# Kernel tuning notes

Hardware: AMD Instinct MI355X
Metric: run time of the kernel (lower is better)

## Reference

```python
import jax, jax.numpy as jnp
import numpy as np

NUM_LEVELS = 16
LEVEL_DIM = 2
BASE_RES = 16
END_RES = 2048
TABLE = 1 << 19  # log2_hashmap_size = 19
DIVIDE = 1.5
FV = 256  # feature_vector_size
H = 256   # hidden width
N = 262144
_scale = np.exp((np.log(END_RES) - np.log(BASE_RES)) / (NUM_LEVELS - 1))
RES = [int(np.ceil(BASE_RES * _scale ** l)) for l in range(NUM_LEVELS)]


def hash_encode(x, tables):
    # x: [N,3], assumed in [-1,1]; map to [0,1] as instant-ngp does
    x01 = jnp.clip((x + 1.0) * 0.5, 0.0, 1.0)
    feats = []
    for l in range(NUM_LEVELS):
        res = RES[l]
        pos = x01 * (res - 1)                      # [N,3]
        p0 = jnp.floor(pos).astype(jnp.int32)
        w = pos - p0                               # trilinear weights
        dense = (res + 1) ** 3 <= TABLE            # static per level
        acc = jnp.zeros((x.shape[0], LEVEL_DIM), x.dtype)
        for c in range(8):                         # 8 cube corners
            off = np.array([(c >> d) & 1 for d in range(3)], dtype=np.int32)
            p = jnp.minimum(p0 + off, res)
            if dense:
                idx = p[:, 0] + (res + 1) * (p[:, 1] + (res + 1) * p[:, 2])
            else:
                pu = p.astype(jnp.uint32)
                idx = (pu[:, 0] ^ (pu[:, 1] * np.uint32(2654435761)) ^ (pu[:, 2] * np.uint32(805459861))) & np.uint32(TABLE - 1)
                idx = idx.astype(jnp.int32)
            wc = jnp.prod(jnp.where(off == 1, w, 1.0 - w), axis=-1, keepdims=True)
            acc = acc + wc * tables[l][idx]
        feats.append(acc)
    return jnp.concatenate(feats, -1)              # [N, 32]


def softplus100(x):
    # torch.nn.Softplus(beta=100)
    return jnp.logaddexp(0.0, 100.0 * x) / 100.0


def mlp(h, W0, b0, W1, b1, W2, b2):
    h = softplus100(h @ W0.T + b0)
    h = softplus100(h @ W1.T + b1)
    return h @ W2.T + b2


def setup_inputs() -> dict:
    key = jax.random.key(0)
    ks = jax.random.split(key, 12)
    GF = NUM_LEVELS * LEVEL_DIM
    d_c = 3 + GF           # coarse MLP input dim (35)
    d_f = 3 + GF + FV      # fine MLP input dim (291)

    def w(k, o, i):
        return jax.random.normal(k, (o, i), jnp.float32) * np.float32(1.0 / np.sqrt(i))

    return {
        'x': jax.random.uniform(ks[0], (N, 3), jnp.float32, -1.0, 1.0),
        'c_tables': jax.random.normal(ks[1], (NUM_LEVELS, TABLE, LEVEL_DIM), jnp.float32) * 1e-2,
        'c_W0': w(ks[2], H, d_c), 'c_b0': jnp.zeros((H,), jnp.float32),
        'c_W1': w(ks[3], H, H),   'c_b1': jnp.zeros((H,), jnp.float32),
        'c_W2': w(ks[4], 1 + FV, H), 'c_b2': jnp.zeros((1 + FV,), jnp.float32),
        'f_tables': jax.random.normal(ks[5], (NUM_LEVELS, TABLE, LEVEL_DIM), jnp.float32) * 1e-2,
        'f_W0': w(ks[6], H, d_f), 'f_b0': jnp.zeros((H,), jnp.float32),
        'f_W1': w(ks[7], H, H),   'f_b1': jnp.zeros((H,), jnp.float32),
        'f_W2': w(ks[8], 1 + FV, H), 'f_b2': jnp.zeros((1 + FV,), jnp.float32),
    }


def reference(x, c_tables, c_W0, c_b0, c_W1, c_b1, c_W2, c_b2,
              f_tables, f_W0, f_b0, f_W1, f_b1, f_W2, f_b2):
    # coarse network: input = [x, hash_feat]
    c_feat = hash_encode(x / DIVIDE, c_tables)
    c_in = jnp.concatenate([x, c_feat], -1)
    c_out = mlp(c_in, c_W0, c_b0, c_W1, c_b1, c_W2, c_b2)  # [N, 1+FV]
    c_fv = c_out[:, 1:]
    # fine network with concat_coarse_feature: input = [x, hash_feat, c_fv]
    f_feat = hash_encode(x / DIVIDE, f_tables)
    f_in = jnp.concatenate([x, f_feat, c_fv], -1)
    f_out = mlp(f_in, f_W0, f_b0, f_W1, f_b1, f_W2, f_b2)  # [N, 1+FV]
    # COMBINE: (c_sdf + f_sdf, c_feature + f_feature) == c_out + f_out
    return c_out + f_out
```

## Files before the change

### kernel.cpp

```cpp
#include <hip/hip_runtime.h>
#include <cmath>

#define NLEV 16
#define TBLSZ 524288
#define TMASK 524287u
#define STR 66
#define ROWS 291
#define NPB 64

typedef short short8 __attribute__((ext_vector_type(8)));
typedef float f32x4 __attribute__((ext_vector_type(4)));
typedef unsigned int u32;
typedef unsigned short u16;

struct EncParams { int res[NLEV]; unsigned dense_mask; };

__device__ __host__ __forceinline__ u32 bf16_rtne_bits(float x) {
  union { float f; u32 u; } c; c.f = x;
  return (c.u + 0x7fffu + ((c.u >> 16) & 1u)) >> 16;
}

__device__ __forceinline__ float softplus100(float x) {
  float t = 100.0f * x;
  return (fmaxf(t, 0.0f) + log1pf(expf(-fabsf(t)))) * 0.01f;
}

__device__ __forceinline__ u32 pack_hl(float x) {
  u32 hi = bf16_rtne_bits(x);
  float r = x - __uint_as_float(hi << 16);
  u32 lo = bf16_rtne_bits(r);
  return hi | (lo << 16);
}

struct AF { short8 h, l; };

template<int KT, int IN>
__device__ __forceinline__ void load_a(const u32* hb, int p, int kq, AF* af) {
  #pragma unroll
  for (int t = 0; t < KT; ++t) {
    u32 pk[8];
    const bool tail = ((t + 1) * 32 > IN);
    #pragma unroll
    for (int e = 0; e < 8; ++e) {
      const int k = t * 32 + kq + e;
      if (tail) {
        const int row = (k < IN) ? k : (IN - 1);
        const u32 v = hb[row * STR + p];
        pk[e] = (k < IN) ? v : 0u;
      } else {
        pk[e] = hb[k * STR + p];
      }
    }
    union { u32 u[4]; short8 v; } ch, cl;
    #pragma unroll
    for (int q = 0; q < 4; ++q) {
      ch.u[q] = __builtin_amdgcn_perm(pk[2 * q + 1], pk[2 * q], 0x05040100u);
      cl.u[q] = __builtin_amdgcn_perm(pk[2 * q + 1], pk[2 * q], 0x07060302u);
    }
    af[t].h = ch.v;
    af[t].l = cl.v;
  }
}

template<int KT, int NT, int IN, class Post>
__device__ __forceinline__ void layer(const u32* __restrict__ hb,
                                      const u16* __restrict__ wf,
                                      const float* __restrict__ bias,
                                      int p, int kq, int l, Post&& post) {
  AF af[KT];
  load_a<KT, IN>(hb, p, kq, af);
  __syncthreads();
  const short8* __restrict__ wp0 = ((const short8*)wf) + (l << 1);
  #pragma unroll 2
  for (int n = 0; n < NT; ++n) {
    const int j = n * 16 + (l & 15);
    const float bv = bias[j];
    f32x4 acc = {bv, bv, bv, bv};
    const short8* wp = wp0 + (size_t)(n * KT) * 128;
    #pragma unroll
    for (int t = 0; t < KT; ++t) {
      const short8 bh = wp[t * 128];
      const short8 bl = wp[t * 128 + 1];
      acc = __builtin_amdgcn_mfma_f32_16x16x32_bf16(af[t].h, bh, acc, 0, 0, 0);
      acc = __builtin_amdgcn_mfma_f32_16x16x32_bf16(af[t].h, bl, acc, 0, 0, 0);
      acc = __builtin_amdgcn_mfma_f32_16x16x32_bf16(af[t].l, bh, acc, 0, 0, 0);
    }
    post(n, j, acc);
  }
}

__global__ __launch_bounds__(256)
void prep_weights(const float* __restrict__ s0, const float* __restrict__ s1,
                  const float* __restrict__ s2, const float* __restrict__ s3,
                  const float* __restrict__ s4, const float* __restrict__ s5,
                  u16* __restrict__ ws) {
  const int O[6]   = {256, 256, 257, 256, 256, 257};
  const int K[6]   = {35, 256, 256, 291, 256, 256};
  const int KT[6]  = {2, 8, 8, 10, 8, 8};
  const int NE[6]  = {16384, 65536, 69632, 81920, 65536, 69632};
  const int OFF[6] = {0, 32768, 163840, 303104, 466944, 598016};
  const float* S[6] = {s0, s1, s2, s3, s4, s5};
  int t = blockIdx.x * 256 + threadIdx.x;
  #pragma unroll
  for (int L = 0; L < 6; ++L) {
    if (t < NE[L]) {
      const int e = t & 7, lane = (t >> 3) & 63, f = t >> 9;
      const int kt = f % KT[L], nt = f / KT[L];
      const int j = nt * 16 + (lane & 15);
      const int k = kt * 32 + ((lane >> 4) << 3) + e;
      const float v = (j < O[L] && k < K[L]) ? S[L][(size_t)j * K[L] + k] : 0.0f;
      const u32 hi = bf16_rtne_bits(v);
      const float r = v - __uint_as_float(hi << 16);
      const u32 lo = bf16_rtne_bits(r);
      u16* d = ws + OFF[L] + (size_t)f * 1024 + (size_t)lane * 16;
      d[e] = (u16)hi;
      d[8 + e] = (u16)lo;
      return;
    }
    t -= NE[L];
  }
}

__global__ __launch_bounds__(256, 2)
void fused_ingp(const float* __restrict__ x,
                const float* __restrict__ ctab, const float* __restrict__ cb0,
                const float* __restrict__ cb1, const float* __restrict__ cb2,
                const float* __restrict__ ftab, const float* __restrict__ fb0,
                const float* __restrict__ fb1, const float* __restrict__ fb2,
                const u16* __restrict__ cW0p, const u16* __restrict__ cW1p,
                const u16* __restrict__ cW2p, const u16* __restrict__ fW0p,
                const u16* __restrict__ fW1p, const u16* __restrict__ fW2p,
                float* __restrict__ out, EncParams ep) {
  __shared__ u32 hb[ROWS * STR];
  const int tid = threadIdx.x;
  const int l = tid & 63;
  const int g = __builtin_amdgcn_readfirstlane(tid >> 6);
  const int pbase = blockIdx.x * NPB;
  const int pt = pbase + l;
  const int p = g * 16 + (l & 15);
  const int kq = (l >> 4) << 3;
  const int colb = g * 16 + ((l >> 4) << 2);

  const float* xp = x + (size_t)3 * pt;
  const float x0 = xp[0], x1 = xp[1], x2 = xp[2];
  const float q0 = fminf(fmaxf((x0 / 1.5f + 1.0f) * 0.5f, 0.0f), 1.0f);
  const float q1 = fminf(fmaxf((x1 / 1.5f + 1.0f) * 0.5f, 0.0f), 1.0f);
  const float q2 = fminf(fmaxf((x2 / 1.5f + 1.0f) * 0.5f, 0.0f), 1.0f);

  if (g == 0) {
    const u32 px0 = pack_hl(x0), px1 = pack_hl(x1), px2 = pack_hl(x2);
    hb[0 * STR + l] = px0; hb[1 * STR + l] = px1; hb[2 * STR + l] = px2;
    hb[288 * STR + l] = px0; hb[289 * STR + l] = px1; hb[290 * STR + l] = px2;
  }

  #pragma unroll
  for (int il = 0; il < 4; ++il) {
    const int lv = g * 4 + il;
    const int res = ep.res[lv];
    const bool dense = (ep.dense_mask >> lv) & 1;
    const float rf = (float)(res - 1);
    const float px = q0 * rf, py = q1 * rf, pz = q2 * rf;
    const int ix = (int)floorf(px), iy = (int)floorf(py), iz = (int)floorf(pz);
    const float wx = px - (float)ix, wy = py - (float)iy, wz = pz - (float)iz;
    float ca0 = 0.f, ca1 = 0.f, fa0 = 0.f, fa1 = 0.f;
    const float* ct = ctab + (size_t)lv * TBLSZ * 2;
    const float* ft = ftab + (size_t)lv * TBLSZ * 2;
    #pragma unroll
    for (int c = 0; c < 8; ++c) {
      const int ox = c & 1, oy = (c >> 1) & 1, oz = (c >> 2) & 1;
      const int cx = min(ix + ox, res), cy = min(iy + oy, res), cz = min(iz + oz, res);
      unsigned idx;
      if (dense) idx = (unsigned)(cx + (res + 1) * (cy + (res + 1) * cz));
      else idx = (((unsigned)cx) ^ ((unsigned)cy * 2654435761u) ^ ((unsigned)cz * 805459861u)) & TMASK;
      const float wc = (ox ? wx : 1.0f - wx) * (oy ? wy : 1.0f - wy) * (oz ? wz : 1.0f - wz);
      const float2 cv = *(const float2*)(ct + (size_t)idx * 2);
      const float2 fv = *(const float2*)(ft + (size_t)idx * 2);
      ca0 = fmaf(wc, cv.x, ca0); ca1 = fmaf(wc, cv.y, ca1);
      fa0 = fmaf(wc, fv.x, fa0); fa1 = fmaf(wc, fv.y, fa1);
    }
    hb[(3 + 2 * lv) * STR + l] = pack_hl(ca0);
    hb[(4 + 2 * lv) * STR + l] = pack_hl(ca1);
    hb[(256 + 2 * lv) * STR + l] = pack_hl(fa0);
    hb[(257 + 2 * lv) * STR + l] = pack_hl(fa1);
  }
  __syncthreads();

  auto post_act = [&](int n, int j, f32x4 a) {
    (void)n;
    #pragma unroll
    for (int r = 0; r < 4; ++r)
      hb[j * STR + colb + r] = pack_hl(softplus100(a[r]));
  };

  layer<2, 16, 35>(hb, cW0p, cb0, p, kq, l, post_act);
  __syncthreads();
  layer<8, 16, 256>(hb, cW1p, cb1, p, kq, l, post_act);
  __syncthreads();

  f32x4 ck[17];
  {
    AF af[8];
    load_a<8, 256>(hb, p, kq, af);
    __syncthreads();
    for (int r = g; r < 35; r += 4) {
      const int src = (r < 3) ? (288 + r) : (253 + r);
      hb[r * STR + l] = hb[src * STR + l];
    }
    __syncthreads();
    const short8* __restrict__ wp0 = ((const short8*)cW2p) + (l << 1);
    #pragma unroll
    for (int n = 0; n < 17; ++n) {
      const int j = n * 16 + (l & 15);
      const float bv = (j < 257) ? cb2[j] : 0.0f;
      f32x4 a = {bv, bv, bv, bv};
      const short8* wp = wp0 + (size_t)(n * 8) * 128;
      #pragma unroll
      for (int t = 0; t < 8; ++t) {
        const short8 bh = wp[t * 128];
        const short8 bl = wp[t * 128 + 1];
        a = __builtin_amdgcn_mfma_f32_16x16x32_bf16(af[t].h, bh, a, 0, 0, 0);
        a = __builtin_amdgcn_mfma_f32_16x16x32_bf16(af[t].h, bl, a, 0, 0, 0);
        a = __builtin_amdgcn_mfma_f32_16x16x32_bf16(af[t].l, bh, a, 0, 0, 0);
      }
      ck[n] = a;
      if (j >= 1 && j <= 256) {
        #pragma unroll
        for (int r = 0; r < 4; ++r)
          hb[(34 + j) * STR + colb + r] = pack_hl(a[r]);
      }
    }
  }
  __syncthreads();

  layer<10, 16, 291>(hb, fW0p, fb0, p, kq, l, post_act);
  __syncthreads();
  layer<8, 16, 256>(hb, fW1p, fb1, p, kq, l, post_act);
  __syncthreads();

  {
    AF af[8];
    load_a<8, 256>(hb, p, kq, af);
    __syncthreads();
    float* hbf = (float*)hb;
    const short8* __restrict__ wp0 = ((const short8*)fW2p) + (l << 1);
    #pragma unroll
    for (int n = 0; n < 17; ++n) {
      const int j = n * 16 + (l & 15);
      const float bv = (j < 257) ? fb2[j] : 0.0f;
      f32x4 a = {bv, bv, bv, bv};
      const short8* wp = wp0 + (size_t)(n * 8) * 128;
      #pragma unroll
      for (int t = 0; t < 8; ++t) {
        const short8 bh = wp[t * 128];
        const short8 bl = wp[t * 128 + 1];
        a = __builtin_amdgcn_mfma_f32_16x16x32_bf16(af[t].h, bh, a, 0, 0, 0);
        a = __builtin_amdgcn_mfma_f32_16x16x32_bf16(af[t].h, bl, a, 0, 0, 0);
        a = __builtin_amdgcn_mfma_f32_16x16x32_bf16(af[t].l, bh, a, 0, 0, 0);
      }
      if (j <= 256) {
        #pragma unroll
        for (int r = 0; r < 4; ++r)
          hbf[j * STR + colb + r] = ck[n][r] + a[r];
      }
    }
  }
  __syncthreads();

  const float* hbf = (const float*)hb;
  const size_t obase = (size_t)pbase * 257;
  for (int idx = tid; idx < NPB * 257; idx += 256) {
    const int pp = idx / 257;
    const int j = idx - pp * 257;
    out[obase + idx] = hbf[j * STR + pp];
  }
}

extern "C" void kernel_launch(void* const* d_in, const int* in_sizes, int n_in,
                              void* d_out, int out_size, void* d_ws, size_t ws_size,
                              hipStream_t stream) {
  (void)n_in; (void)out_size; (void)ws_size;
  EncParams ep;
  const double sc = std::exp((std::log(2048.0) - std::log(16.0)) / 15.0);
  unsigned dm = 0;
  for (int l = 0; l < NLEV; ++l) {
    const int r = (int)std::ceil(16.0 * std::pow(sc, (double)l));
    ep.res[l] = r;
    const long long rp = (long long)r + 1;
    if (rp * rp * rp <= (long long)TBLSZ) dm |= (1u << l);
  }
  ep.dense_mask = dm;

  const float* X    = (const float*)d_in[0];
  const float* ctab = (const float*)d_in[1];
  const float* cW0  = (const float*)d_in[2];
  const float* cb0  = (const float*)d_in[3];
  const float* cW1  = (const float*)d_in[4];
  const float* cb1  = (const float*)d_in[5];
  const float* cW2  = (const float*)d_in[6];
  const float* cb2  = (const float*)d_in[7];
  const float* ftab = (const float*)d_in[8];
  const float* fW0  = (const float*)d_in[9];
  const float* fb0  = (const float*)d_in[10];
  const float* fW1  = (const float*)d_in[11];
  const float* fb1  = (const float*)d_in[12];
  const float* fW2  = (const float*)d_in[13];
  const float* fb2  = (const float*)d_in[14];

  u16* ws = (u16*)d_ws;
  u16* cW0p = ws + 0;
  u16* cW1p = ws + 32768;
  u16* cW2p = ws + 163840;
  u16* fW0p = ws + 303104;
  u16* fW1p = ws + 466944;
  u16* fW2p = ws + 598016;

  prep_weights<<<dim3(1440), dim3(256), 0, stream>>>(cW0, cW1, cW2, fW0, fW1, fW2, ws);

  const int N = in_sizes[0] / 3;
  fused_ingp<<<dim3(N / NPB), dim3(256), 0, stream>>>(
      X, ctab, cb0, cb1, cb2, ftab, fb0, fb1, fb2,
      cW0p, cW1p, cW2p, fW0p, fW1p, fW2p,
      (float*)d_out, ep);
}
```

Baseline: 2.327 ms.

## Split MLP tiles 2x2 across waves and spill coarse outputs to global

Each of the four waves now computes 32 points by half of the output columns, instead of 16 points by all columns. Each B-weight fragment is therefore reused across two A tiles, which halves weight loads per MFMA. The coarse output previously lived in a 17-entry register array (ck). It is now packed as hi/lo bf16 into the output buffer with nontemporal stores and read back at the final combine, which lowers register pressure. The cost is an extra global write and read of the coarse result, and a slightly lossy hi/lo bf16 round trip for the coarse output.

```diff
diff --git a/kernel.cpp b/kernel.cpp
--- a/kernel.cpp
+++ b/kernel.cpp
@@ -30,6 +30,9 @@
   float r = x - __uint_as_float(hi << 16);
   u32 lo = bf16_rtne_bits(r);
   return hi | (lo << 16);
+}
+__device__ __forceinline__ float unpack_hl(u32 v) {
+  return __uint_as_float(v << 16) + __uint_as_float(v & 0xFFFF0000u);
 }
 
 struct AF { short8 h, l; };
@@ -62,30 +65,35 @@
   }
 }
 
-template<int KT, int NT, int IN, class Post>
-__device__ __forceinline__ void layer(const u32* __restrict__ hb,
-                                      const u16* __restrict__ wf,
-                                      const float* __restrict__ bias,
-                                      int p, int kq, int l, Post&& post) {
-  AF af[KT];
-  load_a<KT, IN>(hb, p, kq, af);
+template<int KT, int NTW, int IN, class Post>
+__device__ __forceinline__ void layer2(const u32* __restrict__ hb,
+                                       const u16* __restrict__ wf,
+                                       const float* __restrict__ bias,
+                                       int nbase, int p0, int kq, int l, Post&& post) {
+  AF a0[KT], a1[KT];
+  load_a<KT, IN>(hb, p0, kq, a0);
+  load_a<KT, IN>(hb, p0 + 16, kq, a1);
   __syncthreads();
   const short8* __restrict__ wp0 = ((const short8*)wf) + (l << 1);
   #pragma unroll 2
-  for (int n = 0; n < NT; ++n) {
-    const int j = n * 16 + (l & 15);
+  for (int n = 0; n < NTW; ++n) {
+    const int nn = nbase + n;
+    const int j = nn * 16 + (l & 15);
     const float bv = bias[j];
-    f32x4 acc = {bv, bv, bv, bv};
-    const short8* wp = wp0 + (size_t)(n * KT) * 128;
+    f32x4 acc0 = {bv, bv, bv, bv}, acc1 = acc0;
+    const short8* wp = wp0 + (size_t)(nn * KT) * 128;
     #pragma unroll
     for (int t = 0; t < KT; ++t) {
       const short8 bh = wp[t * 128];
       const short8 bl = wp[t * 128 + 1];
-      acc = __builtin_amdgcn_mfma_f32_16x16x32_bf16(af[t].h, bh, acc, 0, 0, 0);
-      acc = __builtin_amdgcn_mfma_f32_16x16x32_bf16(af[t].h, bl, acc, 0, 0, 0);
-      acc = __builtin_amdgcn_mfma_f32_16x16x32_bf16(af[t].l, bh, acc, 0, 0, 0);
-    }
-    post(n, j, acc);
+      acc0 = __builtin_amdgcn_mfma_f32_16x16x32_bf16(a0[t].h, bh, acc0, 0, 0, 0);
+      acc1 = __builtin_amdgcn_mfma_f32_16x16x32_bf16(a1[t].h, bh, acc1, 0, 0, 0);
+      acc0 = __builtin_amdgcn_mfma_f32_16x16x32_bf16(a0[t].h, bl, acc0, 0, 0, 0);
+      acc1 = __builtin_amdgcn_mfma_f32_16x16x32_bf16(a1[t].h, bl, acc1, 0, 0, 0);
+      acc0 = __builtin_amdgcn_mfma_f32_16x16x32_bf16(a0[t].l, bh, acc0, 0, 0, 0);
+      acc1 = __builtin_amdgcn_mfma_f32_16x16x32_bf16(a1[t].l, bh, acc1, 0, 0, 0);
+    }
+    post(j, acc0, acc1);
   }
 }
 
@@ -135,11 +143,13 @@
   const int tid = threadIdx.x;
   const int l = tid & 63;
   const int g = __builtin_amdgcn_readfirstlane(tid >> 6);
+  const int mg = g & 1;
+  const int ng = g >> 1;
   const int pbase = blockIdx.x * NPB;
   const int pt = pbase + l;
-  const int p = g * 16 + (l & 15);
+  const int p0 = mg * 32 + (l & 15);
   const int kq = (l >> 4) << 3;
-  const int colb = g * 16 + ((l >> 4) << 2);
+  const int cb = mg * 32 + ((l >> 4) << 2);
 
   const float* xp = x + (size_t)3 * pt;
   const float x0 = xp[0], x1 = xp[1], x2 = xp[2];
@@ -185,22 +195,24 @@
   }
   __syncthreads();
 
-  auto post_act = [&](int n, int j, f32x4 a) {
-    (void)n;
-    #pragma unroll
-    for (int r = 0; r < 4; ++r)
-      hb[j * STR + colb + r] = pack_hl(softplus100(a[r]));
+  auto post_act = [&](int j, f32x4 a0, f32x4 a1) {
+    #pragma unroll
+    for (int r = 0; r < 4; ++r) {
+      hb[j * STR + cb + r]      = pack_hl(softplus100(a0[r]));
+      hb[j * STR + cb + 16 + r] = pack_hl(softplus100(a1[r]));
+    }
   };
 
-  layer<2, 16, 35>(hb, cW0p, cb0, p, kq, l, post_act);
-  __syncthreads();
-  layer<8, 16, 256>(hb, cW1p, cb1, p, kq, l, post_act);
-  __syncthreads();
-
-  f32x4 ck[17];
+  layer2<2, 8, 35>(hb, cW0p, cb0, ng * 8, p0, kq, l, post_act);
+  __syncthreads();
+  layer2<8, 8, 256>(hb, cW1p, cb1, ng * 8, p0, kq, l, post_act);
+  __syncthreads();
+
+  u32* __restrict__ out_u = (u32*)out;
   {
-    AF af[8];
-    load_a<8, 256>(hb, p, kq, af);
+    AF a0[8], a1[8];
+    load_a<8, 256>(hb, p0, kq, a0);
+    load_a<8, 256>(hb, p0 + 16, kq, a1);
     __syncthreads();
     for (int r = g; r < 35; r += 4) {
       const int src = (r < 3) ? (288 + r) : (253 + r);
@@ -208,59 +220,77 @@
     }
     __syncthreads();
     const short8* __restrict__ wp0 = ((const short8*)cW2p) + (l << 1);
-    #pragma unroll
-    for (int n = 0; n < 17; ++n) {
-      const int j = n * 16 + (l & 15);
+    const int NTW = ng ? 8 : 9, nb = ng ? 9 : 0;
+    for (int n = 0; n < NTW; ++n) {
+      const int nn = nb + n;
+      const int j = nn * 16 + (l & 15);
       const float bv = (j < 257) ? cb2[j] : 0.0f;
-      f32x4 a = {bv, bv, bv, bv};
-      const short8* wp = wp0 + (size_t)(n * 8) * 128;
+      f32x4 acc0 = {bv, bv, bv, bv}, acc1 = acc0;
+      const short8* wp = wp0 + (size_t)(nn * 8) * 128;
       #pragma unroll
       for (int t = 0; t < 8; ++t) {
         const short8 bh = wp[t * 128];
         const short8 bl = wp[t * 128 + 1];
-        a = __builtin_amdgcn_mfma_f32_16x16x32_bf16(af[t].h, bh, a, 0, 0, 0);
-        a = __builtin_amdgcn_mfma_f32_16x16x32_bf16(af[t].h, bl, a, 0, 0, 0);
-        a = __builtin_amdgcn_mfma_f32_16x16x32_bf16(af[t].l, bh, a, 0, 0, 0);
-      }
-      ck[n] = a;
-      if (j >= 1 && j <= 256) {
+        acc0 = __builtin_amdgcn_mfma_f32_16x16x32_bf16(a0[t].h, bh, acc0, 0, 0, 0);
+        acc1 = __builtin_amdgcn_mfma_f32_16x16x32_bf16(a1[t].h, bh, acc1, 0, 0, 0);
+        acc0 = __builtin_amdgcn_mfma_f32_16x16x32_bf16(a0[t].h, bl, acc0, 0, 0, 0);
+        acc1 = __builtin_amdgcn_mfma_f32_16x16x32_bf16(a1[t].h, bl, acc1, 0, 0, 0);
+        acc0 = __builtin_amdgcn_mfma_f32_16x16x32_bf16(a0[t].l, bh, acc0, 0, 0, 0);
+        acc1 = __builtin_amdgcn_mfma_f32_16x16x32_bf16(a1[t].l, bh, acc1, 0, 0, 0);
+      }
+      if (j <= 256) {
         #pragma unroll
-        for (int r = 0; r < 4; ++r)
-          hb[(34 + j) * STR + colb + r] = pack_hl(a[r]);
-      }
-    }
-  }
-  __syncthreads();
-
-  layer<10, 16, 291>(hb, fW0p, fb0, p, kq, l, post_act);
-  __syncthreads();
-  layer<8, 16, 256>(hb, fW1p, fb1, p, kq, l, post_act);
+        for (int r = 0; r < 4; ++r) {
+          const u32 v0 = pack_hl(acc0[r]);
+          const u32 v1 = pack_hl(acc1[r]);
+          __builtin_nontemporal_store(v0, &out_u[(size_t)(pbase + cb + r) * 257 + j]);
+          __builtin_nontemporal_store(v1, &out_u[(size_t)(pbase + cb + 16 + r) * 257 + j]);
+          if (j >= 1) {
+            hb[(34 + j) * STR + cb + r]      = v0;
+            hb[(34 + j) * STR + cb + 16 + r] = v1;
+          }
+        }
+      }
+    }
+  }
+  __syncthreads();
+
+  layer2<10, 8, 291>(hb, fW0p, fb0, ng * 8, p0, kq, l, post_act);
+  __syncthreads();
+  layer2<8, 8, 256>(hb, fW1p, fb1, ng * 8, p0, kq, l, post_act);
   __syncthreads();
 
   {
-    AF af[8];
-    load_a<8, 256>(hb, p, kq, af);
+    AF a0[8], a1[8];
+    load_a<8, 256>(hb, p0, kq, a0);
+    load_a<8, 256>(hb, p0 + 16, kq, a1);
     __syncthreads();
     float* hbf = (float*)hb;
     const short8* __restrict__ wp0 = ((const short8*)fW2p) + (l << 1);
-    #pragma unroll
-    for (int n = 0; n < 17; ++n) {
-      const int j = n * 16 + (l & 15);
+    const int NTW = ng ? 8 : 9, nb = ng ? 9 : 0;
+    for (int n = 0; n < NTW; ++n) {
+      const int nn = nb + n;
+      const int j = nn * 16 + (l & 15);
       const float bv = (j < 257) ? fb2[j] : 0.0f;
-      f32x4 a = {bv, bv, bv, bv};
-      const short8* wp = wp0 + (size_t)(n * 8) * 128;
+      f32x4 acc0 = {bv, bv, bv, bv}, acc1 = acc0;
+      const short8* wp = wp0 + (size_t)(nn * 8) * 128;
       #pragma unroll
       for (int t = 0; t < 8; ++t) {
         const short8 bh = wp[t * 128];
         const short8 bl = wp[t * 128 + 1];
-        a = __builtin_amdgcn_mfma_f32_16x16x32_bf16(af[t].h, bh, a, 0, 0, 0);
-        a = __builtin_amdgcn_mfma_f32_16x16x32_bf16(af[t].h, bl, a, 0, 0, 0);
-        a = __builtin_amdgcn_mfma_f32_16x16x32_bf16(af[t].l, bh, a, 0, 0, 0);
+        acc0 = __builtin_amdgcn_mfma_f32_16x16x32_bf16(a0[t].h, bh, acc0, 0, 0, 0);
+        acc1 = __builtin_amdgcn_mfma_f32_16x16x32_bf16(a1[t].h, bh, acc1, 0, 0, 0);
+        acc0 = __builtin_amdgcn_mfma_f32_16x16x32_bf16(a0[t].h, bl, acc0, 0, 0, 0);
+        acc1 = __builtin_amdgcn_mfma_f32_16x16x32_bf16(a1[t].h, bl, acc1, 0, 0, 0);
+        acc0 = __builtin_amdgcn_mfma_f32_16x16x32_bf16(a0[t].l, bh, acc0, 0, 0, 0);
+        acc1 = __builtin_amdgcn_mfma_f32_16x16x32_bf16(a1[t].l, bh, acc1, 0, 0, 0);
       }
       if (j <= 256) {
         #pragma unroll
-        for (int r = 0; r < 4; ++r)
-          hbf[j * STR + colb + r] = ck[n][r] + a[r];
+        for (int r = 0; r < 4; ++r) {
+          hbf[j * STR + cb + r]      = acc0[r];
+          hbf[j * STR + cb + 16 + r] = acc1[r];
+        }
       }
     }
   }
@@ -271,7 +301,8 @@
   for (int idx = tid; idx < NPB * 257; idx += 256) {
     const int pp = idx / 257;
     const int j = idx - pp * 257;
-    out[obase + idx] = hbf[j * STR + pp];
+    const u32 cpk = __builtin_nontemporal_load(&out_u[obase + idx]);
+    out[obase + idx] = unpack_hl(cpk) + hbf[j * STR + pp];
   }
 }
 
```

Result: faster. 2.184 ms (-6.1%).
